# Optimization experiments

Measured on AMD Instinct MI355X. Metric: run time of the kernel, lower is better.

Reference implementation:

```python
import jax, jax.numpy as jnp
import numpy as np

EPS = 1e-5
SCALES = jnp.array([7.0, 7.0, 4.0], dtype=jnp.float32)  # (W, H, T) per source buffer
OUT_T, OUT_H, OUT_W = 3, 5, 5


def _roi_align3d(feat, start, end):
    """feat: [C,T,H,W]; start/end: [3] = (x, y, t). One sample per bin (bin center),
    trilinear interpolation, out-of-bounds -> 0 (standard ROIAlign convention)."""
    C, T, H, W = feat.shape
    dt = feat.dtype

    def centers(s, e, n):
        b = (e - s) / n
        return s + (jnp.arange(n, dtype=dt) + 0.5) * b

    xc = centers(start[0], end[0], OUT_W)  # [Wo]
    yc = centers(start[1], end[1], OUT_H)  # [Ho]
    tc = centers(start[2], end[2], OUT_T)  # [To]

    def prep(c, size):
        valid = ((c >= -1.0) & (c <= size)).astype(dt)
        c = jnp.clip(c, 0.0, size - 1)
        lo = jnp.floor(c).astype(jnp.int32)
        hi = jnp.minimum(lo + 1, size - 1)
        f = c - lo.astype(dt)
        return (lo, hi), ((1.0 - f) * valid, f * valid)

    ti, tw = prep(tc, T)
    yi, yw = prep(yc, H)
    xi, xw = prep(xc, W)

    out = jnp.zeros((C, OUT_T, OUT_H, OUT_W), dtype=dt)
    for a in range(2):
        for b in range(2):
            for c in range(2):
                g = feat[:, ti[a][:, None, None], yi[b][None, :, None], xi[c][None, None, :]]
                w = tw[a][:, None, None] * yw[b][None, :, None] * xw[c][None, None, :]
                out = out + g * w
    return out


def setup_inputs() -> dict:
    key = jax.random.key(0)
    k0, k1, k2 = jax.random.split(key, 3)
    B, C, T, H, W = 128, 1024, 4, 7, 7
    R = 256
    x = jax.random.normal(k0, (B, C, T, H, W), jnp.float32)
    w1 = jax.random.normal(k1, (R, C), jnp.float32) / np.sqrt(C).astype(np.float32)
    w2 = jax.random.normal(k2, (6, R), jnp.float32) / np.sqrt(R).astype(np.float32)
    return dict(
        x=x, w1=w1,
        g1=jnp.ones((R,), jnp.float32), b1=jnp.zeros((R,), jnp.float32),
        m1=jnp.zeros((R,), jnp.float32), v1=jnp.ones((R,), jnp.float32),
        w2=w2,
        g2=jnp.ones((6,), jnp.float32), b2=jnp.zeros((6,), jnp.float32),
        m2=jnp.zeros((6,), jnp.float32), v2=jnp.ones((6,), jnp.float32),
    )


def reference(x, w1, g1, b1, m1, v1, w2, g2, b2, m2, v2):
    # roi head: conv1x1x1 -> BN(eval) -> HSwish -> global avgpool -> conv1x1x1 -> BN(eval)
    h = jnp.einsum('bcthw,rc->brthw', x, w1)
    s1 = (g1 / jnp.sqrt(v1 + EPS))
    h = (h - m1[None, :, None, None, None]) * s1[None, :, None, None, None] + b1[None, :, None, None, None]
    h = h * jnp.clip(h + 3.0, 0.0, 6.0) * (1.0 / 6.0)  # HSwish
    h = h.mean(axis=(2, 3, 4))                          # AvgPool3d over full (T,H,W) -> [B,R]
    logits = h @ w2.T
    logits = (logits - m2) * (g2 / jnp.sqrt(v2 + EPS)) + b2  # [B,6]
    raw = jax.nn.sigmoid(logits)
    roi_start = 0.5 * raw[:, :3] * SCALES              # (x1,y1,t1)
    roi_end = (1.0 - 0.5 * raw[:, 3:]) * SCALES        # (x2,y2,t2)
    return jax.vmap(_roi_align3d)(x, roi_start, roi_end)  # [B,C,3,5,5]
```

## Files before the change

kernel.cpp:

```cpp
#include <hip/hip_runtime.h>

typedef __bf16 bf16x8 __attribute__((ext_vector_type(8)));
typedef __bf16 bf16x4 __attribute__((ext_vector_type(4)));
typedef float f32x4 __attribute__((ext_vector_type(4)));

#define EPS_F 1e-5f

__global__ __launch_bounds__(512, 8) void k_gemm_pool(
    const float* __restrict__ x,
    const float* __restrict__ w1,
    const float* __restrict__ g1,
    const float* __restrict__ b1,
    const float* __restrict__ m1,
    const float* __restrict__ v1,
    float* __restrict__ pooled_part)
{
    constexpr int LDK = 40;
    __shared__ __bf16 Alds[112 * LDK];
    __shared__ __bf16 Blds[64 * LDK];
    __shared__ float pool_lds[2][64];

    const int b   = blockIdx.x;
    const int r0  = blockIdx.y * 64;
    const int mc  = blockIdx.z;
    const int tid = threadIdx.x;
    const int wave = tid >> 6, lane = tid & 63;
    const int wm = wave >> 2, wn = wave & 3;
    const int q  = lane >> 4, ln = lane & 15;
    const int nm = (wm == 0) ? 4 : 3;

    f32x4 acc[4];
#pragma unroll
    for (int i = 0; i < 4; i++) acc[i] = (f32x4){0.f, 0.f, 0.f, 0.f};

    const int c4  = tid & 7;
    const int p4  = tid >> 3;
    const bool a_act = (p4 < 28);
    const int  pg    = mc * 28 + p4;
    const bool a_val = a_act && (pg < 49);
    const float* xb = x + (size_t)b * 1024 * 196 + pg * 4;

    const int rB = tid >> 3, k16 = tid & 7;

    for (int kc = 0; kc < 1024; kc += 32) {
        __syncthreads();
        {
            const float4 f = *(const float4*)(w1 + (size_t)(r0 + rB) * 1024 + kc + k16 * 4);
            bf16x4 o = {(__bf16)f.x, (__bf16)f.y, (__bf16)f.z, (__bf16)f.w};
            *(bf16x4*)&Blds[rB * LDK + k16 * 4] = o;
        }
        if (a_act) {
            float fv[4][4];
            if (a_val) {
#pragma unroll
                for (int i = 0; i < 4; i++) {
                    const float4 f = *(const float4*)(xb + (size_t)(kc + c4 * 4 + i) * 196);
                    fv[i][0] = f.x; fv[i][1] = f.y; fv[i][2] = f.z; fv[i][3] = f.w;
                }
            } else {
#pragma unroll
                for (int i = 0; i < 4; i++)
#pragma unroll
                    for (int j = 0; j < 4; j++) fv[i][j] = 0.f;
            }
#pragma unroll
            for (int j = 0; j < 4; j++) {
                bf16x4 o = {(__bf16)fv[0][j], (__bf16)fv[1][j],
                            (__bf16)fv[2][j], (__bf16)fv[3][j]};
                *(bf16x4*)&Alds[(p4 * 4 + j) * LDK + c4 * 4] = o;
            }
        }
        __syncthreads();
        const bf16x8 bfr = *(const bf16x8*)&Blds[(wn * 16 + ln) * LDK + q * 8];
#pragma unroll
        for (int mi = 0; mi < 4; mi++) {
            if (mi < nm) {
                const int mt = wm * 4 + mi;
                const bf16x8 af = *(const bf16x8*)&Alds[(mt * 16 + ln) * LDK + q * 8];
                acc[mi] = __builtin_amdgcn_mfma_f32_16x16x32_bf16(af, bfr, acc[mi], 0, 0, 0);
            }
        }
    }

    float psum = 0.f;
    {
        const int r = r0 + wn * 16 + ln;
        const float s1 = g1[r] * rsqrtf(v1[r] + EPS_F);
        const float mu = m1[r];
        const float be = b1[r];
#pragma unroll
        for (int mi = 0; mi < 4; mi++) {
            if (mi < nm) {
                const int mt = wm * 4 + mi;
#pragma unroll
                for (int i = 0; i < 4; i++) {
                    const int m = mc * 112 + mt * 16 + q * 4 + i;
                    if (m < 196) {
                        float v = acc[mi][i];
                        v = (v - mu) * s1 + be;
                        const float g = fminf(fmaxf(v + 3.f, 0.f), 6.f);
                        psum += v * g * (1.f / 6.f);
                    }
                }
            }
        }
    }
    psum += __shfl_xor(psum, 16, 64);
    psum += __shfl_xor(psum, 32, 64);
    if (lane < 16) pool_lds[wm][wn * 16 + lane] = psum;
    __syncthreads();
    if (tid < 64)
        pooled_part[(size_t)mc * (128 * 256) + b * 256 + r0 + tid] =
            (pool_lds[0][tid] + pool_lds[1][tid]) * (1.f / 196.f);
}

__global__ __launch_bounds__(64) void k_logits(
    const float* __restrict__ pooled_part,
    const float* __restrict__ w2,
    const float* __restrict__ g2,
    const float* __restrict__ b2,
    const float* __restrict__ m2,
    const float* __restrict__ v2,
    float* __restrict__ roi)
{
    const int b = blockIdx.x, t = threadIdx.x;
    const float4 pa = ((const float4*)(pooled_part + b * 256))[t];
    const float4 pb = ((const float4*)(pooled_part + 128 * 256 + b * 256))[t];
    float4 p4;
    p4.x = pa.x + pb.x; p4.y = pa.y + pb.y;
    p4.z = pa.z + pb.z; p4.w = pa.w + pb.w;
    float part[6];
#pragma unroll
    for (int j = 0; j < 6; j++) {
        const float4 w = *(const float4*)(w2 + j * 256 + t * 4);
        part[j] = p4.x * w.x + p4.y * w.y + p4.z * w.z + p4.w * w.w;
    }
#pragma unroll
    for (int j = 0; j < 6; j++)
#pragma unroll
        for (int off = 32; off >= 1; off >>= 1)
            part[j] += __shfl_xor(part[j], off, 64);
    if (t == 0) {
        const float SC[3] = {7.f, 7.f, 4.f};
        float raw[6];
#pragma unroll
        for (int j = 0; j < 6; j++) {
            float l = part[j];
            const float s = g2[j] * rsqrtf(v2[j] + EPS_F);
            l = (l - m2[j]) * s + b2[j];
            raw[j] = 1.f / (1.f + expf(-l));
        }
#pragma unroll
        for (int d = 0; d < 3; d++) {
            roi[b * 6 + d]     = 0.5f * raw[d] * SC[d];
            roi[b * 6 + 3 + d] = (1.f - 0.5f * raw[3 + d]) * SC[d];
        }
    }
}

__device__ __forceinline__ void prep1(float s, float e, int n, int size, int i,
                                      int& lo, int& hi, float& w0, float& w1)
{
    const float bsz = (e - s) / (float)n;
    float c = s + ((float)i + 0.5f) * bsz;
    const float valid = (c >= -1.f && c <= (float)size) ? 1.f : 0.f;
    c = fminf(fmaxf(c, 0.f), (float)(size - 1));
    lo = (int)floorf(c);
    hi = min(lo + 1, size - 1);
    const float f = c - (float)lo;
    w0 = (1.f - f) * valid;
    w1 = f * valid;
}

__global__ __launch_bounds__(256) void k_roi(
    const float* __restrict__ x,
    const float* __restrict__ roi,
    float* __restrict__ out)
{
    __shared__ float xs[32 * 200];
    __shared__ int   soff[8][80];
    __shared__ float swt[8][80];

    const int b = blockIdx.x, c0 = blockIdx.y * 32;
    const int tid = threadIdx.x;

    const float* xb = x + ((size_t)b * 1024 + c0) * 196;
#pragma unroll
    for (int k = 0; k < 7; k++) {
        const int i4 = tid + k * 256;
        if (i4 < 1568) {
            const int c = i4 / 49, pq = i4 % 49;
            const float4 v = *(const float4*)(xb + c * 196 + pq * 4);
            *(float4*)&xs[c * 200 + pq * 4] = v;
        }
    }
    if (tid < 75) {
        const int po = tid;
        const int to = po / 25, rem = po % 25, yo = rem / 5, xo = rem % 5;
        const float sx = roi[b * 6 + 0], ex = roi[b * 6 + 3];
        const float sy = roi[b * 6 + 1], ey = roi[b * 6 + 4];
        const float st = roi[b * 6 + 2], et = roi[b * 6 + 5];
        int tl, th, yl, yh, xl, xh;
        float tw0, tw1, yw0, yw1, xw0, xw1;
        prep1(st, et, 3, 4, to, tl, th, tw0, tw1);
        prep1(sy, ey, 5, 7, yo, yl, yh, yw0, yw1);
        prep1(sx, ex, 5, 7, xo, xl, xh, xw0, xw1);
#pragma unroll
        for (int s = 0; s < 8; s++) {
            const int   ti = (s & 4) ? th : tl;
            const int   yi = (s & 2) ? yh : yl;
            const int   xi = (s & 1) ? xh : xl;
            const float w = ((s & 4) ? tw1 : tw0) *
                            ((s & 2) ? yw1 : yw0) *
                            ((s & 1) ? xw1 : xw0);
            soff[s][po] = ti * 49 + yi * 7 + xi;
            swt[s][po]  = w;
        }
    }
    __syncthreads();

    const size_t obase = ((size_t)b * 1024 + c0) * 75;
#pragma unroll
    for (int k = 0; k < 10; k++) {
        const int e = tid + k * 256;
        if (e < 2400) {
            const int c = e / 75, po = e % 75;
            const float* row = &xs[c * 200];
            float v = 0.f;
#pragma unroll
            for (int s = 0; s < 8; s++)
                v += swt[s][po] * row[soff[s][po]];
            out[obase + e] = v;
        }
    }
}

extern "C" void kernel_launch(void* const* d_in, const int* in_sizes, int n_in,
                              void* d_out, int out_size, void* d_ws, size_t ws_size,
                              hipStream_t stream)
{
    const float* x  = (const float*)d_in[0];
    const float* w1 = (const float*)d_in[1];
    const float* g1 = (const float*)d_in[2];
    const float* b1 = (const float*)d_in[3];
    const float* m1 = (const float*)d_in[4];
    const float* v1 = (const float*)d_in[5];
    const float* w2 = (const float*)d_in[6];
    const float* g2 = (const float*)d_in[7];
    const float* b2 = (const float*)d_in[8];
    const float* m2 = (const float*)d_in[9];
    const float* v2 = (const float*)d_in[10];

    float* pooled_part = (float*)d_ws;
    float* roi         = pooled_part + 2 * 128 * 256;
    float* out         = (float*)d_out;

    k_gemm_pool<<<dim3(128, 4, 2), 512, 0, stream>>>(x, w1, g1, b1, m1, v1, pooled_part);
    k_logits<<<128, 64, 0, stream>>>(pooled_part, w2, g2, b2, m2, v2, roi);
    k_roi<<<dim3(128, 32), 256, 0, stream>>>(x, roi, out);
}
```

Before: 244.8 us.

## Compute all 256 R channels per block and prefetch next K chunk into registers

Each GEMM block now covers the full 256-wide R dimension instead of a 64-wide slice, so the x tile for a batch/position chunk is loaded and converted once rather than four times. Global loads for the next K chunk are issued into registers before the MFMA work of the current chunk, overlapping memory latency with compute. The cost is a 4x smaller grid (256 blocks), larger LDS and 16 accumulator tiles per wave, which raises register pressure and may reduce latency hiding.

```diff
diff --git a/kernel.cpp b/kernel.cpp
--- a/kernel.cpp
+++ b/kernel.cpp
@@ -6,7 +6,7 @@
 
 #define EPS_F 1e-5f
 
-__global__ __launch_bounds__(512, 8) void k_gemm_pool(
+__global__ __launch_bounds__(512) void k_gemm_pool(
     const float* __restrict__ x,
     const float* __restrict__ w1,
     const float* __restrict__ g1,
@@ -17,100 +17,133 @@
 {
     constexpr int LDK = 40;
     __shared__ __bf16 Alds[112 * LDK];
-    __shared__ __bf16 Blds[64 * LDK];
-    __shared__ float pool_lds[2][64];
+    __shared__ __bf16 Blds[256 * LDK];
+    __shared__ float pool_lds[2][256];
 
     const int b   = blockIdx.x;
-    const int r0  = blockIdx.y * 64;
-    const int mc  = blockIdx.z;
+    const int mc  = blockIdx.y;
     const int tid = threadIdx.x;
     const int wave = tid >> 6, lane = tid & 63;
     const int wm = wave >> 2, wn = wave & 3;
     const int q  = lane >> 4, ln = lane & 15;
     const int nm = (wm == 0) ? 4 : 3;
 
-    f32x4 acc[4];
-#pragma unroll
-    for (int i = 0; i < 4; i++) acc[i] = (f32x4){0.f, 0.f, 0.f, 0.f};
+    f32x4 acc[4][4];
+#pragma unroll
+    for (int i = 0; i < 4; i++)
+#pragma unroll
+        for (int j = 0; j < 4; j++) acc[i][j] = (f32x4){0.f, 0.f, 0.f, 0.f};
 
     const int c4  = tid & 7;
     const int p4  = tid >> 3;
     const bool a_act = (p4 < 28);
     const int  pg    = mc * 28 + p4;
     const bool a_val = a_act && (pg < 49);
-    const float* xb = x + (size_t)b * 1024 * 196 + pg * 4;
-
-    const int rB = tid >> 3, k16 = tid & 7;
+    const float* xb = x + (size_t)b * (1024 * 196) + pg * 4;
+
+    const int rB = tid & 255, kh = tid >> 8;
+    const float* wrow = w1 + (size_t)rB * 1024 + kh * 16;
+
+    float  fA[4][4];
+    float4 fB[4];
+
+    auto loadA = [&](int kc) {
+        if (a_val) {
+#pragma unroll
+            for (int i = 0; i < 4; i++) {
+                const float4 f = *(const float4*)(xb + (size_t)(kc + c4 * 4 + i) * 196);
+                fA[i][0] = f.x; fA[i][1] = f.y; fA[i][2] = f.z; fA[i][3] = f.w;
+            }
+        } else {
+#pragma unroll
+            for (int i = 0; i < 4; i++)
+#pragma unroll
+                for (int j = 0; j < 4; j++) fA[i][j] = 0.f;
+        }
+    };
+    auto loadB = [&](int kc) {
+#pragma unroll
+        for (int j = 0; j < 4; j++)
+            fB[j] = *(const float4*)(wrow + kc + j * 4);
+    };
+
+    loadB(0);
+    if (a_act) loadA(0);
 
     for (int kc = 0; kc < 1024; kc += 32) {
         __syncthreads();
         {
-            const float4 f = *(const float4*)(w1 + (size_t)(r0 + rB) * 1024 + kc + k16 * 4);
-            bf16x4 o = {(__bf16)f.x, (__bf16)f.y, (__bf16)f.z, (__bf16)f.w};
-            *(bf16x4*)&Blds[rB * LDK + k16 * 4] = o;
+            bf16x8 lo = {(__bf16)fB[0].x, (__bf16)fB[0].y, (__bf16)fB[0].z, (__bf16)fB[0].w,
+                         (__bf16)fB[1].x, (__bf16)fB[1].y, (__bf16)fB[1].z, (__bf16)fB[1].w};
+            bf16x8 hi = {(__bf16)fB[2].x, (__bf16)fB[2].y, (__bf16)fB[2].z, (__bf16)fB[2].w,
+                         (__bf16)fB[3].x, (__bf16)fB[3].y, (__bf16)fB[3].z, (__bf16)fB[3].w};
+            *(bf16x8*)&Blds[rB * LDK + kh * 16]     = lo;
+            *(bf16x8*)&Blds[rB * LDK + kh * 16 + 8] = hi;
         }
         if (a_act) {
-            float fv[4][4];
-            if (a_val) {
-#pragma unroll
-                for (int i = 0; i < 4; i++) {
-                    const float4 f = *(const float4*)(xb + (size_t)(kc + c4 * 4 + i) * 196);
-                    fv[i][0] = f.x; fv[i][1] = f.y; fv[i][2] = f.z; fv[i][3] = f.w;
-                }
-            } else {
-#pragma unroll
-                for (int i = 0; i < 4; i++)
-#pragma unroll
-                    for (int j = 0; j < 4; j++) fv[i][j] = 0.f;
-            }
 #pragma unroll
             for (int j = 0; j < 4; j++) {
-                bf16x4 o = {(__bf16)fv[0][j], (__bf16)fv[1][j],
-                            (__bf16)fv[2][j], (__bf16)fv[3][j]};
+                bf16x4 o = {(__bf16)fA[0][j], (__bf16)fA[1][j],
+                            (__bf16)fA[2][j], (__bf16)fA[3][j]};
                 *(bf16x4*)&Alds[(p4 * 4 + j) * LDK + c4 * 4] = o;
             }
         }
+        if (kc + 32 < 1024) {
+            loadB(kc + 32);
+            if (a_act) loadA(kc + 32);
+        }
         __syncthreads();
-        const bf16x8 bfr = *(const bf16x8*)&Blds[(wn * 16 + ln) * LDK + q * 8];
+        bf16x8 bfr[4];
+#pragma unroll
+        for (int ni = 0; ni < 4; ni++)
+            bfr[ni] = *(const bf16x8*)&Blds[((wn * 4 + ni) * 16 + ln) * LDK + q * 8];
 #pragma unroll
         for (int mi = 0; mi < 4; mi++) {
             if (mi < nm) {
-                const int mt = wm * 4 + mi;
-                const bf16x8 af = *(const bf16x8*)&Alds[(mt * 16 + ln) * LDK + q * 8];
-                acc[mi] = __builtin_amdgcn_mfma_f32_16x16x32_bf16(af, bfr, acc[mi], 0, 0, 0);
-            }
-        }
-    }
-
-    float psum = 0.f;
-    {
-        const int r = r0 + wn * 16 + ln;
+                const bf16x8 af = *(const bf16x8*)&Alds[((wm * 4 + mi) * 16 + ln) * LDK + q * 8];
+#pragma unroll
+                for (int ni = 0; ni < 4; ni++)
+                    acc[mi][ni] = __builtin_amdgcn_mfma_f32_16x16x32_bf16(af, bfr[ni], acc[mi][ni], 0, 0, 0);
+            }
+        }
+    }
+
+    float psum[4] = {0.f, 0.f, 0.f, 0.f};
+#pragma unroll
+    for (int ni = 0; ni < 4; ni++) {
+        const int r = (wn * 4 + ni) * 16 + ln;
         const float s1 = g1[r] * rsqrtf(v1[r] + EPS_F);
         const float mu = m1[r];
         const float be = b1[r];
 #pragma unroll
         for (int mi = 0; mi < 4; mi++) {
             if (mi < nm) {
-                const int mt = wm * 4 + mi;
 #pragma unroll
                 for (int i = 0; i < 4; i++) {
-                    const int m = mc * 112 + mt * 16 + q * 4 + i;
+                    const int m = mc * 112 + (wm * 4 + mi) * 16 + q * 4 + i;
                     if (m < 196) {
-                        float v = acc[mi][i];
+                        float v = acc[mi][ni][i];
                         v = (v - mu) * s1 + be;
                         const float g = fminf(fmaxf(v + 3.f, 0.f), 6.f);
-                        psum += v * g * (1.f / 6.f);
+                        psum[ni] += v * g * (1.f / 6.f);
                     }
                 }
             }
         }
     }
-    psum += __shfl_xor(psum, 16, 64);
-    psum += __shfl_xor(psum, 32, 64);
-    if (lane < 16) pool_lds[wm][wn * 16 + lane] = psum;
+#pragma unroll
+    for (int ni = 0; ni < 4; ni++) {
+        psum[ni] += __shfl_xor(psum[ni], 16, 64);
+        psum[ni] += __shfl_xor(psum[ni], 32, 64);
+    }
+    if (lane < 16) {
+#pragma unroll
+        for (int ni = 0; ni < 4; ni++)
+            pool_lds[wm][(wn * 4 + ni) * 16 + lane] = psum[ni];
+    }
     __syncthreads();
-    if (tid < 64)
-        pooled_part[(size_t)mc * (128 * 256) + b * 256 + r0 + tid] =
+    if (tid < 256)
+        pooled_part[(size_t)mc * (128 * 256) + b * 256 + tid] =
             (pool_lds[0][tid] + pool_lds[1][tid]) * (1.f / 196.f);
 }
 
@@ -255,7 +288,7 @@
     float* roi         = pooled_part + 2 * 128 * 256;
     float* out         = (float*)d_out;
 
-    k_gemm_pool<<<dim3(128, 4, 2), 512, 0, stream>>>(x, w1, g1, b1, m1, v1, pooled_part);
+    k_gemm_pool<<<dim3(128, 2), 512, 0, stream>>>(x, w1, g1, b1, m1, v1, pooled_part);
     k_logits<<<128, 64, 0, stream>>>(pooled_part, w2, g2, b2, m2, v2, roi);
     k_roi<<<dim3(128, 32), 256, 0, stream>>>(x, roi, out);
 }
```

Measured after the change: 241.6 us. No clear change (-1.3%).
